# Kernel tuning notes

Hardware: AMD Instinct MI355X
Metric: run time of the kernel (lower is better)

## Reference

```python
import jax, jax.numpy as jnp
from jax import lax
import numpy as np

B, DIM, H, W = 1, 48, 192, 192
HEADS, K, DIL = 2, 7, 3
HD = DIM // HEADS
HID = int(DIM * 2.66)  # 127 (Restormer GEGLU hidden)
EPS = 1e-5


def _window_starts(L, Kk, D):
    # NATTEN window-start rule: keep phase i % D, shift window inside bounds.
    s = np.zeros(L, dtype=np.int32)
    for i in range(L):
        if D <= 1:
            st = max(i - Kk // 2, 0)
            if i + Kk // 2 >= L:
                st = L - Kk
        else:
            st = i - (Kk // 2) * D
            if st < 0:
                st = i % D
            elif i + (Kk // 2) * D >= L:
                imodd = i % D
                a = (L // D) * D
                b = L - a
                if imodd < b:
                    st = L - b + imodd - 2 * (Kk // 2) * D
                else:
                    st = a + imodd - Kk * D
        s[i] = st
    return s


def _nbr_tables(L, Kk, D):
    st = _window_starts(L, Kk, D)
    idx = st[:, None] + np.arange(Kk)[None, :] * D          # [L, K] absolute neighbor idx
    pb = (st - np.arange(L)) // D                            # signed offset of window start (in dilation units)
    pb = pb[:, None] + (Kk - 1) + np.arange(Kk)[None, :]     # [L, K] rpb index in [0, 2K-2]
    return jnp.asarray(idx), jnp.asarray(pb)

IH, PBH = _nbr_tables(H, K, DIL)
IW, PBW = _nbr_tables(W, K, DIL)


def layernorm(x, w, b):  # channel LN on NCHW (WithBias, biased var)
    mu = x.mean(1, keepdims=True)
    var = ((x - mu) ** 2).mean(1, keepdims=True)
    return (x - mu) / jnp.sqrt(var + EPS) * w[None, :, None, None] + b[None, :, None, None]


def na2d(x, qkv_w, qkv_b, rpb, proj_w, proj_b):
    # x: NCHW -> BHWC
    t = x.transpose(0, 2, 3, 1)
    qkv = t @ qkv_w.T + qkv_b                                # [B,H,W,3*DIM]
    qkv = qkv.reshape(B, H, W, 3, HEADS, HD)
    q, k, v = qkv[:, :, :, 0], qkv[:, :, :, 1], qkv[:, :, :, 2]
    q = q * (HD ** -0.5)
    # gather dilated 7x7 neighborhoods: [B, H, K, W, K, heads, hd]
    kn = k[:, IH[:, :, None, None], IW[None, None, :, :]]
    vn = v[:, IH[:, :, None, None], IW[None, None, :, :]]
    attn = jnp.einsum('bijnc,bixjync->bijnxy', q, kn)        # [B,H,W,heads,K,K]
    bias = rpb[:, PBH][:, :, :, PBW]                         # [heads,H,K,W,K]
    attn = attn + bias.transpose(1, 3, 0, 2, 4)
    attn = jax.nn.softmax(attn.reshape(B, H, W, HEADS, K * K), axis=-1)
    attn = attn.reshape(B, H, W, HEADS, K, K)
    out = jnp.einsum('bijnxy,bixjync->bijnc', attn, vn).reshape(B, H, W, DIM)
    out = out @ proj_w.T + proj_b
    return out.transpose(0, 3, 1, 2)


def chan_mod(x, eca_w):  # ECA-style gate: GAP -> 1D conv over channels -> sigmoid
    p = x.mean((2, 3))                                       # [B,C]
    y = lax.conv_general_dilated(p[:, None, :], eca_w[None, None, :], (1,), [(3, 3)],
                                 dimension_numbers=('NCH', 'OIH', 'NCH'))[:, 0, :]
    return jax.nn.sigmoid(y)[:, :, None, None]


def ffn(x, w_in, w_dw, w_out):  # conv-GEGLU
    t = jnp.einsum('bchw,oc->bohw', x, w_in)                 # 1x1: DIM -> 2*HID
    t = lax.conv_general_dilated(t, w_dw, (1, 1), [(1, 1), (1, 1)],
                                 feature_group_count=2 * HID,
                                 dimension_numbers=('NCHW', 'OIHW', 'NCHW'))
    x1, x2 = t[:, :HID], t[:, HID:]
    g = jax.nn.gelu(x1, approximate=False) * x2
    return jnp.einsum('bchw,oc->bohw', g, w_out)             # 1x1: HID -> DIM


def setup_inputs() -> dict:
    key = jax.random.key(0)
    ks = jax.random.split(key, 10)
    d = {
        'x': jax.random.normal(ks[0], (B, DIM, H, W), jnp.float32),
        'ln1_w': jnp.ones((DIM,), jnp.float32),
        'ln1_b': jnp.zeros((DIM,), jnp.float32),
        'qkv_w': jax.random.normal(ks[1], (3 * DIM, DIM), jnp.float32) * 0.05,
        'qkv_b': jnp.zeros((3 * DIM,), jnp.float32),
        'rpb': jax.random.normal(ks[2], (HEADS, 2 * K - 1, 2 * K - 1), jnp.float32) * 0.02,
        'proj_w': jax.random.normal(ks[3], (DIM, DIM), jnp.float32) * 0.05,
        'proj_b': jnp.zeros((DIM,), jnp.float32),
        'eca_w': jax.random.normal(ks[4], (7,), jnp.float32) * 0.1,
        'ln2_w': jnp.ones((DIM,), jnp.float32),
        'ln2_b': jnp.zeros((DIM,), jnp.float32),
        'w_in': jax.random.normal(ks[5], (2 * HID, DIM), jnp.float32) * 0.05,
        'w_dw': jax.random.normal(ks[6], (2 * HID, 1, 3, 3), jnp.float32) * 0.05,
        'w_out': jax.random.normal(ks[7], (DIM, HID), jnp.float32) * 0.05,
    }
    return d


def reference(x, ln1_w, ln1_b, qkv_w, qkv_b, rpb, proj_w, proj_b, eca_w,
              ln2_w, ln2_b, w_in, w_dw, w_out):
    xn1 = layernorm(x, ln1_w, ln1_b)
    x = x + na2d(xn1, qkv_w, qkv_b, rpb, proj_w, proj_b) * chan_mod(xn1, eca_w)
    x = x + ffn(layernorm(x, ln2_w, ln2_b), w_in, w_dw, w_out)
    return x
```

## Files before the change

### kernel.cpp

```cpp
#include <hip/hip_runtime.h>
#include <hip/hip_bf16.h>
#include <math.h>

#define HW_ (192*192)
#define Wd 192
#define HIDc 127
#define NBLK1 (HW_/64)

#define O_LN1W 0
#define O_QKVW 96
#define O_QKVB 7008
#define O_RPB  7152
#define O_PROJW 7490
#define O_PROJB 9794
#define O_ECA  9842
#define O_LN2W 9849
#define O_WIN  9945
#define O_WDW  22137
#define O_WOUT 24423
#define WTS_LEN 30519

typedef unsigned short ushort_t;
typedef _Float16 half2_t __attribute__((ext_vector_type(2)));

__device__ __forceinline__ float b2f(__hip_bfloat16 v){ return __bfloat162float(v); }
__device__ __forceinline__ float u2f(ushort_t h){ return __uint_as_float(((unsigned)h)<<16); }
__device__ __forceinline__ ushort_t f2u(float f){
    __hip_bfloat16 h = __float2bfloat16(f);
    union { __hip_bfloat16 b; ushort_t u; } c; c.b = h; return c.u;
}
__device__ __forceinline__ void up2(unsigned u, float& a, float& b){
    a = __uint_as_float(u << 16);
    b = __uint_as_float(u & 0xffff0000u);
}
__device__ __forceinline__ unsigned pkh2(float a, float b){
    half2_t h; h[0] = (_Float16)a; h[1] = (_Float16)b;
    union { half2_t h; unsigned u; } c; c.h = h; return c.u;
}
__device__ __forceinline__ half2_t u2h2(unsigned u){
    union { unsigned u; half2_t h; } c; c.u = u; return c.h;
}
__device__ __forceinline__ float dot2h(half2_t a, half2_t b, float c){
    return c + (float)a[0]*(float)b[0] + (float)a[1]*(float)b[1];
}

__device__ __forceinline__ int wstart(int i){
    if (i < 9) return i % 3;
    if (i >= 183) return 171 + (i % 3);
    return i - 9;
}

__device__ __forceinline__ float dot48bf(const uint4* wr, const float* xr){
    float acc = 0.f;
    #pragma unroll
    for (int c8 = 0; c8 < 6; c8++){
        uint4 u = wr[c8];
        float f0,f1,f2,f3,f4,f5,f6,f7;
        up2(u.x,f0,f1); up2(u.y,f2,f3); up2(u.z,f4,f5); up2(u.w,f6,f7);
        acc += f0*xr[8*c8]   + f1*xr[8*c8+1] + f2*xr[8*c8+2] + f3*xr[8*c8+3]
             + f4*xr[8*c8+4] + f5*xr[8*c8+5] + f6*xr[8*c8+6] + f7*xr[8*c8+7];
    }
    return acc;
}

__global__ void convert_kernel(
    const void* p0, const void* p1, const void* p2, const void* p3,
    const void* p4, const void* p5, const void* p6, const void* p7,
    const void* p8, const void* p9, const void* p10, const void* p11,
    const void* p12, const ushort_t* __restrict__ xu, int* __restrict__ mode_out,
    float* __restrict__ wts, ushort_t* __restrict__ qkvbf, ushort_t* __restrict__ woutTbf,
    ushort_t* __restrict__ winbf, ushort_t* __restrict__ projbf)
{
    __shared__ int sbad;
    if (threadIdx.x == 0) sbad = 0;
    __syncthreads();
    {
        unsigned u = xu[2*threadIdx.x];
        float f = __uint_as_float(u << 16);
        if (!(fabsf(f) < 100.f)) atomicAdd(&sbad, 1);
    }
    __syncthreads();
    const int md = (sbad > 16) ? 1 : 0;
    if (blockIdx.x == 0 && threadIdx.x == 0) mode_out[0] = md;

    const void* ps[13] = {p0,p1,p2,p3,p4,p5,p6,p7,p8,p9,p10,p11,p12};
    const int sz[13]  = {48,48,6912,144,338,2304,48,7,48,48,12192,2286,6096};
    const int off[13] = {O_LN1W,48,O_QKVW,O_QKVB,O_RPB,O_PROJW,O_PROJB,O_ECA,
                         O_LN2W,9897,O_WIN,O_WDW,O_WOUT};
    int b = blockIdx.x;
    if (b >= 13){
        if (b == 13){
            if (md){
                const float* s = (const float*)p2;
                for (int i = threadIdx.x; i < 6912; i += 256) qkvbf[i] = f2u(s[i]);
            } else {
                const ushort_t* s = (const ushort_t*)p2;
                for (int i = threadIdx.x; i < 6912; i += 256) qkvbf[i] = s[i];
            }
        } else if (b == 14){
            if (md){
                const float* s = (const float*)p12;
                for (int i = threadIdx.x; i < 6096; i += 256){
                    int c = i / 48, o = i - c*48;
                    woutTbf[i] = f2u(s[o*127 + c]);
                }
            } else {
                const ushort_t* s = (const ushort_t*)p12;
                for (int i = threadIdx.x; i < 6096; i += 256){
                    int c = i / 48, o = i - c*48;
                    woutTbf[i] = s[o*127 + c];
                }
            }
        } else if (b == 15){
            if (md){
                const float* s = (const float*)p10;
                for (int i = threadIdx.x; i < 12192; i += 256) winbf[i] = f2u(s[i]);
            } else {
                const ushort_t* s = (const ushort_t*)p10;
                for (int i = threadIdx.x; i < 12192; i += 256) winbf[i] = s[i];
            }
        } else {
            if (md){
                const float* s = (const float*)p5;
                for (int i = threadIdx.x; i < 2304; i += 256) projbf[i] = f2u(s[i]);
            } else {
                const ushort_t* s = (const ushort_t*)p5;
                for (int i = threadIdx.x; i < 2304; i += 256) projbf[i] = s[i];
            }
        }
        return;
    }
    int n = sz[b];
    float* dst = wts + off[b];
    if (md){
        const float* s = (const float*)ps[b];
        for (int i = threadIdx.x; i < n; i += 256) dst[i] = s[i];
    } else {
        const __hip_bfloat16* s = (const __hip_bfloat16*)ps[b];
        for (int i = threadIdx.x; i < n; i += 256) dst[i] = b2f(s[i]);
    }
}

__global__ __launch_bounds__(384) void ln1qkv_kernel(
    const void* __restrict__ x, const int* __restrict__ mode,
    const float* __restrict__ wts, const ushort_t* __restrict__ qkvbf,
    ushort_t* __restrict__ q, ushort_t* __restrict__ k, ushort_t* __restrict__ v,
    float* __restrict__ chpart)
{
    __shared__ float sx[64*49];

    const int tid  = threadIdx.x;
    const int px_l = tid & 63;
    const int r6   = __builtin_amdgcn_readfirstlane(tid >> 6);
    const int p0   = blockIdx.x * 64;
    const int p    = p0 + px_l;

    if (mode[0]){
        const float* xf = (const float*)x;
        for (int idx = tid; idx < 64*48; idx += 384){
            int c = idx >> 6, pl = idx & 63;
            sx[pl*49 + c] = xf[c*HW_ + p0 + pl];
        }
    } else {
        const __hip_bfloat16* xb = (const __hip_bfloat16*)x;
        for (int idx = tid; idx < 64*48; idx += 384){
            int c = idx >> 6, pl = idx & 63;
            sx[pl*49 + c] = b2f(xb[c*HW_ + p0 + pl]);
        }
    }
    __syncthreads();

    float xr[48];
    float mu = 0.f;
    #pragma unroll
    for (int c = 0; c < 48; c++){ xr[c] = sx[px_l*49 + c]; mu += xr[c]; }
    mu *= (1.f/48.f);
    float var = 0.f;
    #pragma unroll
    for (int c = 0; c < 48; c++){ float d = xr[c]-mu; var += d*d; }
    var *= (1.f/48.f);
    float rs = rsqrtf(var + 1e-5f);
    #pragma unroll
    for (int c = 0; c < 48; c++)
        xr[c] = (xr[c]-mu)*rs*wts[O_LN1W + c] + wts[O_LN1W + 48 + c];

    if (tid < 64){
        #pragma unroll
        for (int c = 0; c < 48; c++){
            float s = xr[c];
            s += __shfl_xor(s, 1);  s += __shfl_xor(s, 2);  s += __shfl_xor(s, 4);
            s += __shfl_xor(s, 8);  s += __shfl_xor(s, 16); s += __shfl_xor(s, 32);
            if (tid == 0) chpart[blockIdx.x*48 + c] = s;
        }
    }

    const int rbase = r6 * 24;
    const float scale = (r6 < 2) ? 0.20412414523193154f : 1.0f;
    float ov[24];
    #pragma unroll 4
    for (int ro = 0; ro < 24; ro++){
        int r = rbase + ro;
        float acc = wts[O_QKVB + r]
                  + dot48bf((const uint4*)(qkvbf + r*48), xr);
        ov[ro] = acc * scale;
    }

    unsigned int pk[12];
    #pragma unroll
    for (int d = 0; d < 12; d++)
        pk[d] = pkh2(ov[2*d], ov[2*d+1]);
    ushort_t* tp = (r6 >> 1) == 0 ? q : ((r6 >> 1) == 1 ? k : v);
    uint4* dst4 = (uint4*)(tp + (size_t)p*48 + (r6 & 1)*24);
    dst4[0] = make_uint4(pk[0], pk[1], pk[2],  pk[3]);
    dst4[1] = make_uint4(pk[4], pk[5], pk[6],  pk[7]);
    dst4[2] = make_uint4(pk[8], pk[9], pk[10], pk[11]);
}

__global__ __launch_bounds__(256) void gatefuse_kernel(
    const float* __restrict__ chpart, const float* __restrict__ wts,
    float* __restrict__ gate)
{
    __shared__ float sm[48];
    const int t = threadIdx.x;
    if (t < 192){
        const int ch = t >> 2, qq = t & 3;
        float acc = 0.f;
        #pragma unroll 4
        for (int b = qq; b < NBLK1; b += 4)
            acc += chpart[b*48 + ch];
        acc += __shfl_xor(acc, 1);
        acc += __shfl_xor(acc, 2);
        if (qq == 0) sm[ch] = acc * (1.f / (float)HW_);
    }
    __syncthreads();
    if (t < 48){
        float a = 0.f;
        for (int kk = 0; kk < 7; kk++){
            int cc = t + kk - 3;
            if (cc >= 0 && cc < 48) a += wts[O_ECA + kk] * sm[cc];
        }
        gate[t] = 1.f / (1.f + expf(-a));
    }
}

__global__ __launch_bounds__(256) void attnfuse_kernel(
    const ushort_t* __restrict__ q, const ushort_t* __restrict__ k,
    const ushort_t* __restrict__ v, const float* __restrict__ wts,
    const ushort_t* __restrict__ projbf, const float* __restrict__ gate,
    const void* __restrict__ x, const int* __restrict__ mode,
    float* __restrict__ x2, const ushort_t* __restrict__ winbf,
    ushort_t* __restrict__ tout)
{
    __shared__ float srpb[338];
    __shared__ float sa[64*49];

    const int tid = threadIdx.x;
    for (int i0 = tid; i0 < 338; i0 += 256) srpb[i0] = wts[O_RPB + i0];
    __syncthreads();

    const int parity = tid & 1;
    const int head   = (tid >> 1) & 1;
    const int px_l   = tid >> 2;
    const int px     = blockIdx.x * 64 + px_l;
    const int i = px / Wd, j = px % Wd;
    const int sti = wstart(i), stj = wstart(j);
    const int pbi = (sti - i) / 3 + 6;
    const int pbj = (stj - j) / 3 + 6;
    const int choff = head * 24;
    const float* rpb = srpb + head*169;

    half2_t qh[12];
    {
        const uint4* qp = (const uint4*)(q + (size_t)px*48 + choff);
        uint4 q0 = qp[0], q1 = qp[1], q2 = qp[2];
        qh[0]=u2h2(q0.x); qh[1]=u2h2(q0.y); qh[2] =u2h2(q0.z); qh[3] =u2h2(q0.w);
        qh[4]=u2h2(q1.x); qh[5]=u2h2(q1.y); qh[6] =u2h2(q1.z); qh[7] =u2h2(q1.w);
        qh[8]=u2h2(q2.x); qh[9]=u2h2(q2.y); qh[10]=u2h2(q2.z); qh[11]=u2h2(q2.w);
    }

    float s = 0.f;
    float acc[24];
    #pragma unroll
    for (int c = 0; c < 24; c++) acc[c] = 0.f;

    #pragma unroll 5
    for (int tt = 0; tt < 25; tt++){
        int n = 2*tt + parity;
        const bool inval = (n > 48);
        if (inval) n = 48;
        int xx = (n * 147) >> 10;
        int yy = n - 7*xx;
        int ii = sti + 3*xx, jj = stj + 3*yy;
        const size_t nb = (size_t)(ii*Wd + jj)*48 + choff;
        const uint4* kp = (const uint4*)(k + nb);
        const uint4* vp = (const uint4*)(v + nb);
        uint4 K0 = kp[0], K1 = kp[1], K2 = kp[2];
        uint4 V0 = vp[0], V1 = vp[1], V2 = vp[2];
        float d = 0.f;
        d = dot2h(u2h2(K0.x), qh[0],  d);
        d = dot2h(u2h2(K0.y), qh[1],  d);
        d = dot2h(u2h2(K0.z), qh[2],  d);
        d = dot2h(u2h2(K0.w), qh[3],  d);
        d = dot2h(u2h2(K1.x), qh[4],  d);
        d = dot2h(u2h2(K1.y), qh[5],  d);
        d = dot2h(u2h2(K1.z), qh[6],  d);
        d = dot2h(u2h2(K1.w), qh[7],  d);
        d = dot2h(u2h2(K2.x), qh[8],  d);
        d = dot2h(u2h2(K2.y), qh[9],  d);
        d = dot2h(u2h2(K2.z), qh[10], d);
        d = dot2h(u2h2(K2.w), qh[11], d);
        float sc = d + rpb[(pbi+xx)*13 + (pbj+yy)];
        sc = fminf(sc, 80.f);
        if (inval) sc = -1e30f;
        float p = __expf(sc);
        s += p;
        half2_t vv;
        vv=u2h2(V0.x); acc[0] +=p*(float)vv[0]; acc[1] +=p*(float)vv[1];
        vv=u2h2(V0.y); acc[2] +=p*(float)vv[0]; acc[3] +=p*(float)vv[1];
        vv=u2h2(V0.z); acc[4] +=p*(float)vv[0]; acc[5] +=p*(float)vv[1];
        vv=u2h2(V0.w); acc[6] +=p*(float)vv[0]; acc[7] +=p*(float)vv[1];
        vv=u2h2(V1.x); acc[8] +=p*(float)vv[0]; acc[9] +=p*(float)vv[1];
        vv=u2h2(V1.y); acc[10]+=p*(float)vv[0]; acc[11]+=p*(float)vv[1];
        vv=u2h2(V1.z); acc[12]+=p*(float)vv[0]; acc[13]+=p*(float)vv[1];
        vv=u2h2(V1.w); acc[14]+=p*(float)vv[0]; acc[15]+=p*(float)vv[1];
        vv=u2h2(V2.x); acc[16]+=p*(float)vv[0]; acc[17]+=p*(float)vv[1];
        vv=u2h2(V2.y); acc[18]+=p*(float)vv[0]; acc[19]+=p*(float)vv[1];
        vv=u2h2(V2.z); acc[20]+=p*(float)vv[0]; acc[21]+=p*(float)vv[1];
        vv=u2h2(V2.w); acc[22]+=p*(float)vv[0]; acc[23]+=p*(float)vv[1];
    }

    s += __shfl_xor(s, 1);
    const float inv = 1.f / s;
    float mg[12];
    #pragma unroll
    for (int c = 0; c < 12; c++){
        float mine   = parity ? acc[12+c] : acc[c];
        float theirs = parity ? acc[c]    : acc[12+c];
        mg[c] = (mine + __shfl_xor(theirs, 1)) * inv;
    }
    {
        float* dst = sa + px_l*49 + choff + parity*12;
        #pragma unroll
        for (int c = 0; c < 12; c++) dst[c] = mg[c];
    }
    __syncthreads();

    const int px_l2 = tid & 63;
    const int og    = __builtin_amdgcn_readfirstlane(tid >> 6);
    const int px2   = blockIdx.x * 64 + px_l2;

    float ar[48];
    #pragma unroll
    for (int c = 0; c < 48; c++) ar[c] = sa[px_l2*49 + c];
    __syncthreads();

    const float* xf = (const float*)x;
    const __hip_bfloat16* xb = (const __hip_bfloat16*)x;
    const int md = mode[0];
    const int ob = og * 12;
    #pragma unroll 2
    for (int oo = 0; oo < 12; oo++){
        int o = ob + oo;
        float accp = wts[O_PROJB + o]
                   + dot48bf((const uint4*)(projbf + o*48), ar);
        float res = md ? xf[o*HW_ + px2] : b2f(xb[o*HW_ + px2]);
        float xv = res + accp * gate[o];
        x2[o*HW_ + px2] = xv;
        sa[px_l2*49 + o] = xv;
    }
    __syncthreads();

    float xr[48];
    float mu = 0.f;
    #pragma unroll
    for (int c = 0; c < 48; c++){ xr[c] = sa[px_l2*49 + c]; mu += xr[c]; }
    mu *= (1.f/48.f);
    float var = 0.f;
    #pragma unroll
    for (int c = 0; c < 48; c++){ float dd = xr[c]-mu; var += dd*dd; }
    var *= (1.f/48.f);
    float rs = rsqrtf(var + 1e-5f);
    #pragma unroll
    for (int c = 0; c < 48; c++)
        xr[c] = (xr[c]-mu)*rs*wts[O_LN2W + c] + wts[O_LN2W + 48 + c];

    const int base = og * 64;
    for (int t2 = 0; t2 < 64; t2 += 2){
        int o0 = base + t2;
        if (o0 >= 254) break;
        const uint4* wA = (const uint4*)(winbf + o0*48);
        const uint4* wB = (const uint4*)(winbf + min(o0+1,253)*48);
        float accA = 0.f, accB = 0.f;
        #pragma unroll
        for (int c8 = 0; c8 < 6; c8++){
            uint4 ua = wA[c8];
            uint4 ub = wB[c8];
            float a0,a1,a2,a3,a4,a5,a6,a7, b0,b1,b2,b3,b4,b5,b6,b7;
            up2(ua.x,a0,a1); up2(ua.y,a2,a3); up2(ua.z,a4,a5); up2(ua.w,a6,a7);
            up2(ub.x,b0,b1); up2(ub.y,b2,b3); up2(ub.z,b4,b5); up2(ub.w,b6,b7);
            accA += a0*xr[8*c8]   + a1*xr[8*c8+1] + a2*xr[8*c8+2] + a3*xr[8*c8+3]
                  + a4*xr[8*c8+4] + a5*xr[8*c8+5] + a6*xr[8*c8+6] + a7*xr[8*c8+7];
            accB += b0*xr[8*c8]   + b1*xr[8*c8+1] + b2*xr[8*c8+2] + b3*xr[8*c8+3]
                  + b4*xr[8*c8+4] + b5*xr[8*c8+5] + b6*xr[8*c8+6] + b7*xr[8*c8+7];
        }
        tout[(size_t)o0*HW_ + px2] = f2u(accA);
        if (o0+1 < 254) tout[(size_t)(o0+1)*HW_ + px2] = f2u(accB);
    }
}

__global__ __launch_bounds__(256) void dw_kernel(
    const ushort_t* __restrict__ t, const float* __restrict__ wts,
    ushort_t* __restrict__ g)
{
    const int ch = blockIdx.y;
    const int pp = (blockIdx.x * 256 + threadIdx.x) * 4;
    const int i  = pp / Wd, j = pp % Wd;
    float w1[9], w2[9];
    #pragma unroll
    for (int s2 = 0; s2 < 9; s2++){
        w1[s2] = wts[O_WDW + ch*9 + s2];
        w2[s2] = wts[O_WDW + (ch+HIDc)*9 + s2];
    }
    const ushort_t* t1 = t + (size_t)ch * HW_;
    const ushort_t* t2 = t + (size_t)(ch+HIDc) * HW_;
    float a10=0.f,a11=0.f,a12=0.f,a13=0.f;
    float a20=0.f,a21=0.f,a22=0.f,a23=0.f;
    #pragma unroll
    for (int di = 0; di < 3; di++){
        int ii = i + di - 1;
        if (ii < 0 || ii >= 192) continue;
        int base = ii*Wd + j;
        float wa = w1[di*3], wb = w1[di*3+1], wc = w1[di*3+2];
        {
            uint2 mm = *(const uint2*)(t1 + base);
            float c0,c1,c2,c3; up2(mm.x,c0,c1); up2(mm.y,c2,c3);
            float cm = (j > 0)     ? u2f(t1[base-1]) : 0.f;
            float cp = (j+4 < Wd)  ? u2f(t1[base+4]) : 0.f;
            a10 += wa*cm + wb*c0 + wc*c1;
            a11 += wa*c0 + wb*c1 + wc*c2;
            a12 += wa*c1 + wb*c2 + wc*c3;
            a13 += wa*c2 + wb*c3 + wc*cp;
        }
        wa = w2[di*3]; wb = w2[di*3+1]; wc = w2[di*3+2];
        {
            uint2 mm = *(const uint2*)(t2 + base);
            float c0,c1,c2,c3; up2(mm.x,c0,c1); up2(mm.y,c2,c3);
            float cm = (j > 0)     ? u2f(t2[base-1]) : 0.f;
            float cp = (j+4 < Wd)  ? u2f(t2[base+4]) : 0.f;
            a20 += wa*cm + wb*c0 + wc*c1;
            a21 += wa*c0 + wb*c1 + wc*c2;
            a22 += wa*c1 + wb*c2 + wc*c3;
            a23 += wa*c2 + wb*c3 + wc*cp;
        }
    }
    const float RS2 = 0.70710678118654752f;
    float g0 = a10 * 0.5f * (1.f + erff(a10 * RS2)) * a20;
    float g1 = a11 * 0.5f * (1.f + erff(a11 * RS2)) * a21;
    float g2 = a12 * 0.5f * (1.f + erff(a12 * RS2)) * a22;
    float g3 = a13 * 0.5f * (1.f + erff(a13 * RS2)) * a23;
    uint2 pk;
    pk.x = (unsigned)f2u(g0) | ((unsigned)f2u(g1) << 16);
    pk.y = (unsigned)f2u(g2) | ((unsigned)f2u(g3) << 16);
    *(uint2*)(g + (size_t)ch*HW_ + pp) = pk;
}

__global__ __launch_bounds__(128) void pw2_kernel(
    const ushort_t* __restrict__ g, const ushort_t* __restrict__ woutTbf,
    const float* __restrict__ x2, void* __restrict__ outv,
    const int* __restrict__ mode)
{
    const int ob = blockIdx.y * 12;
    const int p  = blockIdx.x * 128 + threadIdx.x;
    float acc[12];
    #pragma unroll
    for (int o = 0; o < 12; o++) acc[o] = 0.f;
    #pragma unroll 4
    for (int c = 0; c < 127; c++){
        float gv = u2f(g[(size_t)c*HW_ + p]);
        const unsigned* wr = (const unsigned*)(woutTbf + c*48 + ob);
        #pragma unroll
        for (int d = 0; d < 6; d++){
            float w0, w1;
            up2(wr[d], w0, w1);
            acc[2*d]   += w0*gv;
            acc[2*d+1] += w1*gv;
        }
    }
    if (mode[0]){
        float* out = (float*)outv;
        #pragma unroll
        for (int o = 0; o < 12; o++){
            int oc = ob + o;
            out[(size_t)oc*HW_ + p] = x2[(size_t)oc*HW_ + p] + acc[o];
        }
    } else {
        __hip_bfloat16* out = (__hip_bfloat16*)outv;
        #pragma unroll
        for (int o = 0; o < 12; o++){
            int oc = ob + o;
            out[(size_t)oc*HW_ + p] =
                __float2bfloat16(x2[(size_t)oc*HW_ + p] + acc[o]);
        }
    }
}

extern "C" void kernel_launch(void* const* d_in, const int* in_sizes, int n_in,
                              void* d_out, int out_size, void* d_ws, size_t ws_size,
                              hipStream_t stream)
{
    (void)in_sizes; (void)n_in; (void)out_size;

    char* ws = (char*)d_ws;
    ushort_t* q    = (ushort_t*)(ws);
    ushort_t* k    = (ushort_t*)(ws + 3538944);
    ushort_t* v    = (ushort_t*)(ws + 7077888);
    float*    x2   = (float*)   (ws + 10616832);
    ushort_t* t    = (ushort_t*)(ws + 17694720);
    ushort_t* g    = (ushort_t*)(ws);
    float*    gate = (float*)   (ws + 36421632);
    int*      mode = (int*)     (ws + 36421824);
    float*    wts  = (float*)   (ws + 36421840);
    float*    chpart=(float*)   (ws + 36543920);
    ushort_t* qkvbf   = (ushort_t*)(ws + 36654512);
    ushort_t* woutTbf = (ushort_t*)(ws + 36668336);
    ushort_t* winbf   = (ushort_t*)(ws + 36680528);
    ushort_t* projbf  = (ushort_t*)(ws + 36704912);

    size_t need = 36709520;
    if (ws_size < need) return;

    convert_kernel<<<17, 256, 0, stream>>>(
        d_in[1], d_in[2], d_in[3], d_in[4], d_in[5], d_in[6], d_in[7],
        d_in[8], d_in[9], d_in[10], d_in[11], d_in[12], d_in[13],
        (const ushort_t*)d_in[0], mode, wts, qkvbf, woutTbf, winbf, projbf);

    ln1qkv_kernel<<<dim3(NBLK1), 384, 0, stream>>>(d_in[0], mode, wts, qkvbf,
                                                   q, k, v, chpart);
    gatefuse_kernel<<<1, 256, 0, stream>>>(chpart, wts, gate);
    attnfuse_kernel<<<dim3(HW_/64), 256, 0, stream>>>(q, k, v, wts, projbf, gate,
                                                      d_in[0], mode, x2, winbf, t);
    dw_kernel<<<dim3(HW_/1024, 127), 256, 0, stream>>>(t, wts, g);
    pw2_kernel<<<dim3(HW_/128, 4), 128, 0, stream>>>(g, woutTbf, x2, d_out, mode);
}
```

Baseline: 237.6 us.

## Stage K/V neighborhood rows in shared memory with head-planar QKV layout

The QKV producer now writes q, k and v as separate per-head planes (head-major, 24 channels per pixel) instead of interleaved 48-channel records. The attention kernel processes each head in turn and cooperatively loads the 7 dilated rows by up to 84 columns of K, then of V, into LDS. Each pixel's 4 threads then read their neighbors from LDS instead of issuing scattered global loads. This is meant to cut redundant global and L2 traffic from overlapping neighborhoods, at the cost of extra block barriers, about 28KB more shared memory (which may lower occupancy), and 4-lane shuffle reductions over 24 accumulators.

```diff
diff --git a/kernel.cpp b/kernel.cpp
--- a/kernel.cpp
+++ b/kernel.cpp
@@ -210,7 +210,7 @@
     for (int d = 0; d < 12; d++)
         pk[d] = pkh2(ov[2*d], ov[2*d+1]);
     ushort_t* tp = (r6 >> 1) == 0 ? q : ((r6 >> 1) == 1 ? k : v);
-    uint4* dst4 = (uint4*)(tp + (size_t)p*48 + (r6 & 1)*24);
+    uint4* dst4 = (uint4*)(tp + (size_t)(r6 & 1)*(HW_*24) + (size_t)p*24);
     dst4[0] = make_uint4(pk[0], pk[1], pk[2],  pk[3]);
     dst4[1] = make_uint4(pk[4], pk[5], pk[6],  pk[7]);
     dst4[2] = make_uint4(pk[8], pk[9], pk[10], pk[11]);
@@ -251,97 +251,132 @@
     float* __restrict__ x2, const ushort_t* __restrict__ winbf,
     ushort_t* __restrict__ tout)
 {
+    __shared__ ushort_t skv[7*84*24];
+    __shared__ float sa[64*49];
     __shared__ float srpb[338];
-    __shared__ float sa[64*49];
 
     const int tid = threadIdx.x;
     for (int i0 = tid; i0 < 338; i0 += 256) srpb[i0] = wts[O_RPB + i0];
-    __syncthreads();
-
-    const int parity = tid & 1;
-    const int head   = (tid >> 1) & 1;
-    const int px_l   = tid >> 2;
-    const int px     = blockIdx.x * 64 + px_l;
-    const int i = px / Wd, j = px % Wd;
+
+    const int p4   = tid & 3;
+    const int px_l = tid >> 2;
+    const int p0   = blockIdx.x * 64;
+    const int px   = p0 + px_l;
+    const int i  = px / Wd;
+    const int j  = px % Wd;
+    const int j0 = p0 % Wd;
     const int sti = wstart(i), stj = wstart(j);
+    const int c0  = (j0 > 9) ? (j0 - 9) : 0;
+    int ncols = 192 - c0; if (ncols > 84) ncols = 84;
+    const int ncols3 = ncols * 3;
     const int pbi = (sti - i) / 3 + 6;
     const int pbj = (stj - j) / 3 + 6;
-    const int choff = head * 24;
-    const float* rpb = srpb + head*169;
-
-    half2_t qh[12];
-    {
-        const uint4* qp = (const uint4*)(q + (size_t)px*48 + choff);
-        uint4 q0 = qp[0], q1 = qp[1], q2 = qp[2];
-        qh[0]=u2h2(q0.x); qh[1]=u2h2(q0.y); qh[2] =u2h2(q0.z); qh[3] =u2h2(q0.w);
-        qh[4]=u2h2(q1.x); qh[5]=u2h2(q1.y); qh[6] =u2h2(q1.z); qh[7] =u2h2(q1.w);
-        qh[8]=u2h2(q2.x); qh[9]=u2h2(q2.y); qh[10]=u2h2(q2.z); qh[11]=u2h2(q2.w);
-    }
-
-    float s = 0.f;
-    float acc[24];
-    #pragma unroll
-    for (int c = 0; c < 24; c++) acc[c] = 0.f;
-
-    #pragma unroll 5
-    for (int tt = 0; tt < 25; tt++){
-        int n = 2*tt + parity;
-        const bool inval = (n > 48);
-        if (inval) n = 48;
-        int xx = (n * 147) >> 10;
-        int yy = n - 7*xx;
-        int ii = sti + 3*xx, jj = stj + 3*yy;
-        const size_t nb = (size_t)(ii*Wd + jj)*48 + choff;
-        const uint4* kp = (const uint4*)(k + nb);
-        const uint4* vp = (const uint4*)(v + nb);
-        uint4 K0 = kp[0], K1 = kp[1], K2 = kp[2];
-        uint4 V0 = vp[0], V1 = vp[1], V2 = vp[2];
-        float d = 0.f;
-        d = dot2h(u2h2(K0.x), qh[0],  d);
-        d = dot2h(u2h2(K0.y), qh[1],  d);
-        d = dot2h(u2h2(K0.z), qh[2],  d);
-        d = dot2h(u2h2(K0.w), qh[3],  d);
-        d = dot2h(u2h2(K1.x), qh[4],  d);
-        d = dot2h(u2h2(K1.y), qh[5],  d);
-        d = dot2h(u2h2(K1.z), qh[6],  d);
-        d = dot2h(u2h2(K1.w), qh[7],  d);
-        d = dot2h(u2h2(K2.x), qh[8],  d);
-        d = dot2h(u2h2(K2.y), qh[9],  d);
-        d = dot2h(u2h2(K2.z), qh[10], d);
-        d = dot2h(u2h2(K2.w), qh[11], d);
-        float sc = d + rpb[(pbi+xx)*13 + (pbj+yy)];
-        sc = fminf(sc, 80.f);
-        if (inval) sc = -1e30f;
-        float p = __expf(sc);
-        s += p;
-        half2_t vv;
-        vv=u2h2(V0.x); acc[0] +=p*(float)vv[0]; acc[1] +=p*(float)vv[1];
-        vv=u2h2(V0.y); acc[2] +=p*(float)vv[0]; acc[3] +=p*(float)vv[1];
-        vv=u2h2(V0.z); acc[4] +=p*(float)vv[0]; acc[5] +=p*(float)vv[1];
-        vv=u2h2(V0.w); acc[6] +=p*(float)vv[0]; acc[7] +=p*(float)vv[1];
-        vv=u2h2(V1.x); acc[8] +=p*(float)vv[0]; acc[9] +=p*(float)vv[1];
-        vv=u2h2(V1.y); acc[10]+=p*(float)vv[0]; acc[11]+=p*(float)vv[1];
-        vv=u2h2(V1.z); acc[12]+=p*(float)vv[0]; acc[13]+=p*(float)vv[1];
-        vv=u2h2(V1.w); acc[14]+=p*(float)vv[0]; acc[15]+=p*(float)vv[1];
-        vv=u2h2(V2.x); acc[16]+=p*(float)vv[0]; acc[17]+=p*(float)vv[1];
-        vv=u2h2(V2.y); acc[18]+=p*(float)vv[0]; acc[19]+=p*(float)vv[1];
-        vv=u2h2(V2.z); acc[20]+=p*(float)vv[0]; acc[21]+=p*(float)vv[1];
-        vv=u2h2(V2.w); acc[22]+=p*(float)vv[0]; acc[23]+=p*(float)vv[1];
-    }
-
-    s += __shfl_xor(s, 1);
-    const float inv = 1.f / s;
-    float mg[12];
-    #pragma unroll
-    for (int c = 0; c < 12; c++){
-        float mine   = parity ? acc[12+c] : acc[c];
-        float theirs = parity ? acc[c]    : acc[12+c];
-        mg[c] = (mine + __shfl_xor(theirs, 1)) * inv;
-    }
-    {
-        float* dst = sa + px_l*49 + choff + parity*12;
-        #pragma unroll
-        for (int c = 0; c < 12; c++) dst[c] = mg[c];
+    const int lbase = stj - c0;
+
+    #pragma unroll
+    for (int h = 0; h < 2; h++){
+        half2_t qh[12];
+        {
+            const uint4* qp = (const uint4*)(q + (size_t)h*(HW_*24) + (size_t)px*24);
+            uint4 q0 = qp[0], q1 = qp[1], q2 = qp[2];
+            qh[0]=u2h2(q0.x); qh[1]=u2h2(q0.y); qh[2] =u2h2(q0.z); qh[3] =u2h2(q0.w);
+            qh[4]=u2h2(q1.x); qh[5]=u2h2(q1.y); qh[6] =u2h2(q1.z); qh[7] =u2h2(q1.w);
+            qh[8]=u2h2(q2.x); qh[9]=u2h2(q2.y); qh[10]=u2h2(q2.z); qh[11]=u2h2(q2.w);
+        }
+        __syncthreads();
+        {
+            const uint4* base4 = (const uint4*)(k + (size_t)h*(HW_*24)
+                                     + ((size_t)sti*Wd + c0)*24);
+            if (tid < ncols3){
+                #pragma unroll
+                for (int r = 0; r < 7; r++)
+                    *((uint4*)skv + r*252 + tid) = base4[(size_t)r*1728 + tid];
+            }
+        }
+        __syncthreads();
+
+        float s = 0.f;
+        float p[13];
+        #pragma unroll
+        for (int tt = 0; tt < 13; tt++){
+            int n = 4*tt + p4;
+            const bool bad = (n > 48);
+            if (bad) n = 48;
+            int xx = (n * 147) >> 10;
+            int yy = n - 7*xx;
+            const uint4* rec = (const uint4*)&skv[(xx*84 + lbase + 3*yy)*24];
+            uint4 K0 = rec[0], K1 = rec[1], K2 = rec[2];
+            float d = 0.f;
+            d = dot2h(u2h2(K0.x), qh[0],  d);
+            d = dot2h(u2h2(K0.y), qh[1],  d);
+            d = dot2h(u2h2(K0.z), qh[2],  d);
+            d = dot2h(u2h2(K0.w), qh[3],  d);
+            d = dot2h(u2h2(K1.x), qh[4],  d);
+            d = dot2h(u2h2(K1.y), qh[5],  d);
+            d = dot2h(u2h2(K1.z), qh[6],  d);
+            d = dot2h(u2h2(K1.w), qh[7],  d);
+            d = dot2h(u2h2(K2.x), qh[8],  d);
+            d = dot2h(u2h2(K2.y), qh[9],  d);
+            d = dot2h(u2h2(K2.z), qh[10], d);
+            d = dot2h(u2h2(K2.w), qh[11], d);
+            float sc = d + srpb[h*169 + (pbi+xx)*13 + (pbj+yy)];
+            sc = fminf(sc, 80.f);
+            if (bad) sc = -1e30f;
+            p[tt] = __expf(sc);
+            s += p[tt];
+        }
+        __syncthreads();
+        {
+            const uint4* base4 = (const uint4*)(v + (size_t)h*(HW_*24)
+                                     + ((size_t)sti*Wd + c0)*24);
+            if (tid < ncols3){
+                #pragma unroll
+                for (int r = 0; r < 7; r++)
+                    *((uint4*)skv + r*252 + tid) = base4[(size_t)r*1728 + tid];
+            }
+        }
+        __syncthreads();
+
+        float acc[24];
+        #pragma unroll
+        for (int c = 0; c < 24; c++) acc[c] = 0.f;
+        #pragma unroll
+        for (int tt = 0; tt < 13; tt++){
+            int n = 4*tt + p4;
+            if (n > 48) n = 48;
+            int xx = (n * 147) >> 10;
+            int yy = n - 7*xx;
+            const uint4* rec = (const uint4*)&skv[(xx*84 + lbase + 3*yy)*24];
+            uint4 V0 = rec[0], V1 = rec[1], V2 = rec[2];
+            const float pp = p[tt];
+            half2_t vv;
+            vv=u2h2(V0.x); acc[0] +=pp*(float)vv[0]; acc[1] +=pp*(float)vv[1];
+            vv=u2h2(V0.y); acc[2] +=pp*(float)vv[0]; acc[3] +=pp*(float)vv[1];
+            vv=u2h2(V0.z); acc[4] +=pp*(float)vv[0]; acc[5] +=pp*(float)vv[1];
+            vv=u2h2(V0.w); acc[6] +=pp*(float)vv[0]; acc[7] +=pp*(float)vv[1];
+            vv=u2h2(V1.x); acc[8] +=pp*(float)vv[0]; acc[9] +=pp*(float)vv[1];
+            vv=u2h2(V1.y); acc[10]+=pp*(float)vv[0]; acc[11]+=pp*(float)vv[1];
+            vv=u2h2(V1.z); acc[12]+=pp*(float)vv[0]; acc[13]+=pp*(float)vv[1];
+            vv=u2h2(V1.w); acc[14]+=pp*(float)vv[0]; acc[15]+=pp*(float)vv[1];
+            vv=u2h2(V2.x); acc[16]+=pp*(float)vv[0]; acc[17]+=pp*(float)vv[1];
+            vv=u2h2(V2.y); acc[18]+=pp*(float)vv[0]; acc[19]+=pp*(float)vv[1];
+            vv=u2h2(V2.z); acc[20]+=pp*(float)vv[0]; acc[21]+=pp*(float)vv[1];
+            vv=u2h2(V2.w); acc[22]+=pp*(float)vv[0]; acc[23]+=pp*(float)vv[1];
+        }
+
+        s += __shfl_xor(s, 1);
+        s += __shfl_xor(s, 2);
+        #pragma unroll
+        for (int c = 0; c < 24; c++){
+            acc[c] += __shfl_xor(acc[c], 1);
+            acc[c] += __shfl_xor(acc[c], 2);
+        }
+        if (p4 == 0){
+            const float inv = 1.f / s;
+            #pragma unroll
+            for (int c = 0; c < 24; c++)
+                sa[px_l*49 + h*24 + c] = acc[c] * inv;
+        }
     }
     __syncthreads();
 
```

New measurement: 254.8 us. +7.2%, slower.

## Split fused attention kernel into standalone attention and proj+pw1 kernels

Applied to the files above, without the earlier changes.

The fused attention/projection/LN2/pw1 kernel is split in two. A new attention kernel uses four lanes per pixel per head, with heads on a grid dimension, and writes the bf16 attention output to a new channel-major workspace buffer. A second kernel reads that buffer and does projection, gating, residual, LN2 and the first pointwise conv. The aim is higher occupancy and parallelism in the latency-bound gather loop. The cost is an extra global round trip of about 3.5 MB, one more launch, and a full 24-channel cross-lane reduction.

```diff
diff --git a/kernel.cpp b/kernel.cpp
--- a/kernel.cpp
+++ b/kernel.cpp
@@ -243,31 +243,25 @@
     }
 }
 
-__global__ __launch_bounds__(256) void attnfuse_kernel(
+__global__ __launch_bounds__(128) void attn_kernel(
     const ushort_t* __restrict__ q, const ushort_t* __restrict__ k,
     const ushort_t* __restrict__ v, const float* __restrict__ wts,
-    const ushort_t* __restrict__ projbf, const float* __restrict__ gate,
-    const void* __restrict__ x, const int* __restrict__ mode,
-    float* __restrict__ x2, const ushort_t* __restrict__ winbf,
-    ushort_t* __restrict__ tout)
-{
-    __shared__ float srpb[338];
-    __shared__ float sa[64*49];
-
-    const int tid = threadIdx.x;
-    for (int i0 = tid; i0 < 338; i0 += 256) srpb[i0] = wts[O_RPB + i0];
+    ushort_t* __restrict__ aout)
+{
+    __shared__ float srpb[169];
+    const int head = blockIdx.y;
+    const int tid  = threadIdx.x;
+    for (int i0 = tid; i0 < 169; i0 += 128) srpb[i0] = wts[O_RPB + head*169 + i0];
     __syncthreads();
 
-    const int parity = tid & 1;
-    const int head   = (tid >> 1) & 1;
-    const int px_l   = tid >> 2;
-    const int px     = blockIdx.x * 64 + px_l;
+    const int p4   = tid & 3;
+    const int px_l = tid >> 2;
+    const int px   = blockIdx.x * 32 + px_l;
     const int i = px / Wd, j = px % Wd;
     const int sti = wstart(i), stj = wstart(j);
     const int pbi = (sti - i) / 3 + 6;
     const int pbj = (stj - j) / 3 + 6;
     const int choff = head * 24;
-    const float* rpb = srpb + head*169;
 
     half2_t qh[12];
     {
@@ -283,11 +277,11 @@
     #pragma unroll
     for (int c = 0; c < 24; c++) acc[c] = 0.f;
 
-    #pragma unroll 5
-    for (int tt = 0; tt < 25; tt++){
-        int n = 2*tt + parity;
-        const bool inval = (n > 48);
-        if (inval) n = 48;
+    #pragma unroll 4
+    for (int tt = 0; tt < 13; tt++){
+        int n = 4*tt + p4;
+        const bool bad = (n > 48);
+        if (bad) n = 48;
         int xx = (n * 147) >> 10;
         int yy = n - 7*xx;
         int ii = sti + 3*xx, jj = stj + 3*yy;
@@ -309,9 +303,9 @@
         d = dot2h(u2h2(K2.y), qh[9],  d);
         d = dot2h(u2h2(K2.z), qh[10], d);
         d = dot2h(u2h2(K2.w), qh[11], d);
-        float sc = d + rpb[(pbi+xx)*13 + (pbj+yy)];
+        float sc = d + srpb[(pbi+xx)*13 + (pbj+yy)];
         sc = fminf(sc, 80.f);
-        if (inval) sc = -1e30f;
+        if (bad) sc = -1e30f;
         float p = __expf(sc);
         s += p;
         half2_t vv;
@@ -330,29 +324,49 @@
     }
 
     s += __shfl_xor(s, 1);
+    s += __shfl_xor(s, 2);
+    #pragma unroll
+    for (int c = 0; c < 24; c++){
+        acc[c] += __shfl_xor(acc[c], 1);
+        acc[c] += __shfl_xor(acc[c], 2);
+    }
     const float inv = 1.f / s;
-    float mg[12];
-    #pragma unroll
-    for (int c = 0; c < 12; c++){
-        float mine   = parity ? acc[12+c] : acc[c];
-        float theirs = parity ? acc[c]    : acc[12+c];
-        mg[c] = (mine + __shfl_xor(theirs, 1)) * inv;
-    }
-    {
-        float* dst = sa + px_l*49 + choff + parity*12;
-        #pragma unroll
-        for (int c = 0; c < 12; c++) dst[c] = mg[c];
-    }
-    __syncthreads();
-
-    const int px_l2 = tid & 63;
-    const int og    = __builtin_amdgcn_readfirstlane(tid >> 6);
-    const int px2   = blockIdx.x * 64 + px_l2;
+    if (p4 == 0){
+        #pragma unroll
+        for (int c = 0; c < 6; c++)
+            aout[(size_t)(choff + c)*HW_ + px] = f2u(acc[c] * inv);
+    } else if (p4 == 1){
+        #pragma unroll
+        for (int c = 0; c < 6; c++)
+            aout[(size_t)(choff + 6 + c)*HW_ + px] = f2u(acc[6 + c] * inv);
+    } else if (p4 == 2){
+        #pragma unroll
+        for (int c = 0; c < 6; c++)
+            aout[(size_t)(choff + 12 + c)*HW_ + px] = f2u(acc[12 + c] * inv);
+    } else {
+        #pragma unroll
+        for (int c = 0; c < 6; c++)
+            aout[(size_t)(choff + 18 + c)*HW_ + px] = f2u(acc[18 + c] * inv);
+    }
+}
+
+__global__ __launch_bounds__(256) void projpw1_kernel(
+    const ushort_t* __restrict__ aout, const float* __restrict__ wts,
+    const ushort_t* __restrict__ projbf, const float* __restrict__ gate,
+    const void* __restrict__ x, const int* __restrict__ mode,
+    float* __restrict__ x2, const ushort_t* __restrict__ winbf,
+    ushort_t* __restrict__ tout)
+{
+    __shared__ float sa[64*49];
+
+    const int tid  = threadIdx.x;
+    const int px_l = tid & 63;
+    const int og   = __builtin_amdgcn_readfirstlane(tid >> 6);
+    const int px   = blockIdx.x * 64 + px_l;
 
     float ar[48];
     #pragma unroll
-    for (int c = 0; c < 48; c++) ar[c] = sa[px_l2*49 + c];
-    __syncthreads();
+    for (int c = 0; c < 48; c++) ar[c] = u2f(aout[(size_t)c*HW_ + px]);
 
     const float* xf = (const float*)x;
     const __hip_bfloat16* xb = (const __hip_bfloat16*)x;
@@ -363,17 +377,17 @@
         int o = ob + oo;
         float accp = wts[O_PROJB + o]
                    + dot48bf((const uint4*)(projbf + o*48), ar);
-        float res = md ? xf[o*HW_ + px2] : b2f(xb[o*HW_ + px2]);
+        float res = md ? xf[o*HW_ + px] : b2f(xb[o*HW_ + px]);
         float xv = res + accp * gate[o];
-        x2[o*HW_ + px2] = xv;
-        sa[px_l2*49 + o] = xv;
+        x2[o*HW_ + px] = xv;
+        sa[px_l*49 + o] = xv;
     }
     __syncthreads();
 
     float xr[48];
     float mu = 0.f;
     #pragma unroll
-    for (int c = 0; c < 48; c++){ xr[c] = sa[px_l2*49 + c]; mu += xr[c]; }
+    for (int c = 0; c < 48; c++){ xr[c] = sa[px_l*49 + c]; mu += xr[c]; }
     mu *= (1.f/48.f);
     float var = 0.f;
     #pragma unroll
@@ -403,8 +417,8 @@
             accB += b0*xr[8*c8]   + b1*xr[8*c8+1] + b2*xr[8*c8+2] + b3*xr[8*c8+3]
                   + b4*xr[8*c8+4] + b5*xr[8*c8+5] + b6*xr[8*c8+6] + b7*xr[8*c8+7];
         }
-        tout[(size_t)o0*HW_ + px2] = f2u(accA);
-        if (o0+1 < 254) tout[(size_t)(o0+1)*HW_ + px2] = f2u(accB);
+        tout[(size_t)o0*HW_ + px] = f2u(accA);
+        if (o0+1 < 254) tout[(size_t)(o0+1)*HW_ + px] = f2u(accB);
     }
 }
 
@@ -525,8 +539,9 @@
     ushort_t* woutTbf = (ushort_t*)(ws + 36668336);
     ushort_t* winbf   = (ushort_t*)(ws + 36680528);
     ushort_t* projbf  = (ushort_t*)(ws + 36704912);
-
-    size_t need = 36709520;
+    ushort_t* aout    = (ushort_t*)(ws + 36709520);
+
+    size_t need = 36709520 + 3538944;
     if (ws_size < need) return;
 
     convert_kernel<<<17, 256, 0, stream>>>(
@@ -537,8 +552,9 @@
     ln1qkv_kernel<<<dim3(NBLK1), 384, 0, stream>>>(d_in[0], mode, wts, qkvbf,
                                                    q, k, v, chpart);
     gatefuse_kernel<<<1, 256, 0, stream>>>(chpart, wts, gate);
-    attnfuse_kernel<<<dim3(HW_/64), 256, 0, stream>>>(q, k, v, wts, projbf, gate,
-                                                      d_in[0], mode, x2, winbf, t);
+    attn_kernel<<<dim3(HW_/32, 2), 128, 0, stream>>>(q, k, v, wts, aout);
+    projpw1_kernel<<<dim3(HW_/64), 256, 0, stream>>>(aout, wts, projbf, gate,
+                                                     d_in[0], mode, x2, winbf, t);
     dw_kernel<<<dim3(HW_/1024, 127), 256, 0, stream>>>(t, wts, g);
     pw2_kernel<<<dim3(HW_/128, 4), 128, 0, stream>>>(g, woutTbf, x2, d_out, mode);
 }
```

Result: slower. 246.2 us (+3.6%).
